# Kernel tuning notes

Hardware: AMD Instinct MI355X
Metric: run time of the kernel (lower is better)

Reference implementation:

```python
import jax, jax.numpy as jnp
import numpy as np

D_MODEL = 1024
D_STATE = 32
DT_MIN, DT_MAX = 1e-3, 1e-1
L_LEN = 2048


def setup_inputs() -> dict:
    key = jax.random.key(0)
    k1, k2, k3 = jax.random.split(key, 3)
    # log_dt ~ U[log(dt_min), log(dt_max)]
    log_dt = jax.random.uniform(k1, (D_MODEL,), dtype=jnp.float32) \
        * (np.log(DT_MAX) - np.log(DT_MIN)) + np.log(DT_MIN)
    # log_A_real = log(0.5), A_imag = pi * arange(N) per channel
    log_A_real = jnp.full((D_MODEL, D_STATE), np.log(0.5), dtype=jnp.float32)
    A_imag = jnp.broadcast_to(np.pi * jnp.arange(D_STATE, dtype=jnp.float32),
                              (D_MODEL, D_STATE)).copy()
    # B = 1 + 0j ; C ~ complex normal (real/imag each N(0,1))
    B_re = jnp.ones((D_MODEL, D_STATE), dtype=jnp.float32)
    B_im = jnp.zeros((D_MODEL, D_STATE), dtype=jnp.float32)
    C_re = jax.random.normal(k2, (D_MODEL, D_STATE), dtype=jnp.float32)
    C_im = jax.random.normal(k3, (D_MODEL, D_STATE), dtype=jnp.float32)
    return {"log_dt": log_dt, "log_A_real": log_A_real, "A_imag": A_imag,
            "B_re": B_re, "B_im": B_im, "C_re": C_re, "C_im": C_im,
            "L": L_LEN}


def reference(log_dt, log_A_real, A_imag, B_re, B_im, C_re, C_im, L):
    # ZOH discretization of diagonal SSM, then Vandermonde kernel.
    dt = jnp.exp(log_dt)                                  # (H,)
    A = -jnp.exp(log_A_real) + 1j * A_imag                # (H, N) complex
    dtA = A * dt[:, None]                                 # (H, N)
    A_bar = jnp.exp(dtA)                                  # (H, N)
    B = B_re + 1j * B_im
    C = C_re + 1j * C_im
    B_bar = (A_bar - 1.0) / A * B                         # (H, N)
    t = jnp.arange(L)                                     # (L,)
    # A_bar^t = exp(t * dtA) for integer t (avoids complex pow branch issues,
    # mathematically identical to torch.pow(A_bar, t) here)
    A_bar_pow = jnp.exp(dtA[:, :, None] * t[None, None, :])  # (H, N, L)
    K = jnp.einsum('hn,hnl->hl', C * B_bar, A_bar_pow)       # weighted reduce
    return K.real
```

## Files before the change

kernel.cpp:

```cpp
#include <hip/hip_runtime.h>
#include <hip/hip_bf16.h>

#define H_MODEL 1024
#define N_STATE 32
#define L_LEN   2048
#define BLK     512
#define HALF    256
#define GSTEP   8

__global__ __launch_bounds__(BLK, 8) void s4d_kernel(
    const float* __restrict__ log_dt,
    const float* __restrict__ log_A_real,
    const float* __restrict__ A_imag,
    const float* __restrict__ B_re,
    const float* __restrict__ B_im,
    const float* __restrict__ C_re,
    const float* __restrict__ C_im,
    float* __restrict__ out)
{
    const int h = blockIdx.x;

    __shared__ float4 s_c1[N_STATE];
    __shared__ float4 s_c2[N_STATE];
    __shared__ float  s_part[HALF][GSTEP + 1];

    if (threadIdx.x < N_STATE) {
        const int n   = threadIdx.x;
        const int idx = h * N_STATE + n;
        const float dt   = __expf(log_dt[h]);
        const float a_re = -__expf(log_A_real[idx]);
        const float a_im = A_imag[idx];
        const float dre  = a_re * dt;
        const float dim  = a_im * dt;

        const float er = __expf(dre);
        float sn, cs;
        __sincosf(dim, &sn, &cs);
        const float abar_re = er * cs;
        const float abar_im = er * sn;

        const float num_re = abar_re - 1.0f;
        const float num_im = abar_im;
        const float inv_d  = 1.0f / (a_re * a_re + a_im * a_im);
        const float q_re   = (num_re * a_re + num_im * a_im) * inv_d;
        const float q_im   = (num_im * a_re - num_re * a_im) * inv_d;

        const float br = B_re[idx], bi = B_im[idx];
        const float bb_re = q_re * br - q_im * bi;
        const float bb_im = q_re * bi + q_im * br;
        const float cr = C_re[idx], ci = C_im[idx];
        const float wre = cr * bb_re - ci * bb_im;
        const float wim = cr * bb_im + ci * bb_re;

        const float erB = __expf(dre * (float)HALF);
        float snB, csB;
        __sincosf(dim * (float)HALF, &snB, &csB);
        const float Er = erB * csB;
        const float Ei = erB * snB;
        s_c1[n] = make_float4(dre, dim, wre, wim);
        s_c2[n] = make_float4(Er, Ei, 2.0f * Er, -(Er * Er + Ei * Ei));
    }
    __syncthreads();

    const int  hl    = threadIdx.x >> 8;
    const int  l     = threadIdx.x & (HALF - 1);
    const int  nbase = hl << 4;
    const float t    = (float)l;

    float acc[GSTEP];
    #pragma unroll
    for (int k = 0; k < GSTEP; ++k) acc[k] = 0.0f;

    #pragma unroll 2
    for (int j = 0; j < N_STATE / 2; ++j) {
        const float4 c1 = s_c1[nbase + j];
        const float4 c2 = s_c2[nbase + j];

        const float er = __expf(c1.x * t);
        float sn, cs;
        __sincosf(c1.y * t, &sn, &cs);
        const float z0r = er * (c1.z * cs - c1.w * sn);
        const float z0i = er * (c1.w * cs + c1.z * sn);

        float rp = z0r;
        float rc = z0r * c2.x - z0i * c2.y;
        acc[0] += rp;
        acc[1] += rc;

        #pragma unroll
        for (int k = 2; k < GSTEP; ++k) {
            const float rn = __builtin_fmaf(c2.z, rc, c2.w * rp);
            acc[k] += rn;
            rp = rc; rc = rn;
        }
    }

    if (hl == 1) {
        #pragma unroll
        for (int k = 0; k < GSTEP; ++k) s_part[l][k] = acc[k];
    }
    __syncthreads();
    if (hl == 0) {
        float* orow = out + h * L_LEN + l;
        #pragma unroll
        for (int k = 0; k < GSTEP; ++k)
            orow[k * HALF] = acc[k] + s_part[l][k];
    }
}

extern "C" void kernel_launch(void* const* d_in, const int* in_sizes, int n_in,
                              void* d_out, int out_size, void* d_ws, size_t ws_size,
                              hipStream_t stream) {
    const float* log_dt     = (const float*)d_in[0];
    const float* log_A_real = (const float*)d_in[1];
    const float* A_imag     = (const float*)d_in[2];
    const float* B_re       = (const float*)d_in[3];
    const float* B_im       = (const float*)d_in[4];
    const float* C_re       = (const float*)d_in[5];
    const float* C_im       = (const float*)d_in[6];
    float* out              = (float*)d_out;

    s4d_kernel<<<dim3(H_MODEL), dim3(BLK), 0, stream>>>(
        log_dt, log_A_real, A_imag, B_re, B_im, C_re, C_im, out);
}
```

Baseline: 15.39 us.

## Split states into four groups with packed two-wide stride-2 recurrence

Threads now cover 128 positions, each producing 16 outputs instead of 8, and the 32 states are split across four groups of 8 instead of two groups of 16. The second-order recurrence is rewritten as a stride-2 recurrence on paired values, using packed float2 FMA so two outputs are produced per vector instruction. This cuts the number of exp/sincos evaluations per output and uses packed math. In exchange it adds a three-way shared-memory reduction, more registers for accumulators, and possibly more error growth from longer recurrence chains.

```diff
diff --git a/kernel.cpp b/kernel.cpp
--- a/kernel.cpp
+++ b/kernel.cpp
@@ -5,8 +5,12 @@
 #define N_STATE 32
 #define L_LEN   2048
 #define BLK     512
-#define HALF    256
-#define GSTEP   8
+#define QL      128
+#define GSTEP   16
+#define NPQ     (N_STATE / 4)
+#define NPAIR   (GSTEP / 2)
+
+typedef float v2f __attribute__((ext_vector_type(2)));
 
 __global__ __launch_bounds__(BLK, 8) void s4d_kernel(
     const float* __restrict__ log_dt,
@@ -22,7 +26,7 @@
 
     __shared__ float4 s_c1[N_STATE];
     __shared__ float4 s_c2[N_STATE];
-    __shared__ float  s_part[HALF][GSTEP + 1];
+    __shared__ float  s_part[3][QL][GSTEP + 1];
 
     if (threadIdx.x < N_STATE) {
         const int n   = threadIdx.x;
@@ -52,9 +56,9 @@
         const float wre = cr * bb_re - ci * bb_im;
         const float wim = cr * bb_im + ci * bb_re;
 
-        const float erB = __expf(dre * (float)HALF);
+        const float erB = __expf(dre * (float)QL);
         float snB, csB;
-        __sincosf(dim * (float)HALF, &snB, &csB);
+        __sincosf(dim * (float)QL, &snB, &csB);
         const float Er = erB * csB;
         const float Ei = erB * snB;
         s_c1[n] = make_float4(dre, dim, wre, wim);
@@ -62,19 +66,24 @@
     }
     __syncthreads();
 
-    const int  hl    = threadIdx.x >> 8;
-    const int  l     = threadIdx.x & (HALF - 1);
-    const int  nbase = hl << 4;
-    const float t    = (float)l;
+    const int   q  = threadIdx.x >> 7;
+    const int   l  = threadIdx.x & (QL - 1);
+    const int   nb = q * NPQ;
+    const float t  = (float)l;
 
-    float acc[GSTEP];
+    v2f acc[NPAIR];
     #pragma unroll
-    for (int k = 0; k < GSTEP; ++k) acc[k] = 0.0f;
+    for (int j = 0; j < NPAIR; ++j) acc[j] = (v2f){0.0f, 0.0f};
 
     #pragma unroll 2
-    for (int j = 0; j < N_STATE / 2; ++j) {
-        const float4 c1 = s_c1[nbase + j];
-        const float4 c2 = s_c2[nbase + j];
+    for (int jn = 0; jn < NPQ; ++jn) {
+        const float4 c1 = s_c1[nb + jn];
+        const float4 c2 = s_c2[nb + jn];
+
+        const float a2 = __builtin_fmaf(c2.z, c2.z, c2.w + c2.w);
+        const float b2 = -(c2.w * c2.w);
+        const v2f A2 = {a2, a2};
+        const v2f B2 = {b2, b2};
 
         const float er = __expf(c1.x * t);
         float sn, cs;
@@ -82,29 +91,46 @@
         const float z0r = er * (c1.z * cs - c1.w * sn);
         const float z0i = er * (c1.w * cs + c1.z * sn);
 
-        float rp = z0r;
-        float rc = z0r * c2.x - z0i * c2.y;
-        acc[0] += rp;
-        acc[1] += rc;
+        const float r0 = z0r;
+        const float r1 = z0r * c2.x - z0i * c2.y;
+        const float r2 = __builtin_fmaf(c2.z, r1, c2.w * r0);
+        const float r3 = __builtin_fmaf(c2.z, r2, c2.w * r1);
 
+        v2f P0 = {r0, r1};
+        v2f P1 = {r2, r3};
+        acc[0] += P0;
+        acc[1] += P1;
         #pragma unroll
-        for (int k = 2; k < GSTEP; ++k) {
-            const float rn = __builtin_fmaf(c2.z, rc, c2.w * rp);
-            acc[k] += rn;
-            rp = rc; rc = rn;
+        for (int k = 2; k < NPAIR; ++k) {
+            const v2f Pn = __builtin_elementwise_fma(A2, P1, B2 * P0);
+            acc[k] += Pn;
+            P0 = P1; P1 = Pn;
         }
     }
 
-    if (hl == 1) {
+    if (q != 0) {
         #pragma unroll
-        for (int k = 0; k < GSTEP; ++k) s_part[l][k] = acc[k];
+        for (int j = 0; j < NPAIR; ++j) {
+            s_part[q - 1][l][2 * j]     = acc[j].x;
+            s_part[q - 1][l][2 * j + 1] = acc[j].y;
+        }
     }
     __syncthreads();
-    if (hl == 0) {
+    if (q == 0) {
+        #pragma unroll
+        for (int b = 0; b < 3; ++b) {
+            #pragma unroll
+            for (int j = 0; j < NPAIR; ++j) {
+                acc[j].x += s_part[b][l][2 * j];
+                acc[j].y += s_part[b][l][2 * j + 1];
+            }
+        }
         float* orow = out + h * L_LEN + l;
         #pragma unroll
-        for (int k = 0; k < GSTEP; ++k)
-            orow[k * HALF] = acc[k] + s_part[l][k];
+        for (int j = 0; j < NPAIR; ++j) {
+            orow[(2 * j) * QL]     = acc[j].x;
+            orow[(2 * j + 1) * QL] = acc[j].y;
+        }
     }
 }
 
```

New measurement: 13.50 us. 12.3% less time.
